# Kernel tuning notes

Hardware: AMD Instinct MI355X
Metric: run time of the kernel (lower is better)

## Reference

```python
import jax, jax.numpy as jnp
import numpy as np
import math

B, T, C = 2, 2048, 2048
NH = 16
HS = C // NH            # 128
N_ELEM = int(0.5 * HS)  # 64, rotary_percentage=0.5
A_T = 10                # adapter_prompt_length


def setup_inputs() -> dict:
    key = jax.random.key(0)
    ks = jax.random.split(key, 8)
    x = jax.random.normal(ks[0], (B, T, C), dtype=jnp.float32)
    # RoPE cache: standard cos/sin of shape (T, n_elem)
    theta = 10000.0 ** (-jnp.arange(0, N_ELEM, 2, dtype=jnp.float32) / N_ELEM)
    pos = jnp.arange(T, dtype=jnp.float32)
    ang = pos[:, None] * theta[None, :]           # (T, n_elem/2)
    ang = jnp.concatenate([ang, ang], axis=-1)    # (T, n_elem)
    cos, sin = jnp.cos(ang), jnp.sin(ang)
    mask = jnp.tril(jnp.ones((T, T), dtype=bool))  # causal
    s = 0.02
    attn_w = jax.random.normal(ks[1], (3 * C, C), dtype=jnp.float32) * s
    attn_b = jax.random.normal(ks[2], (3 * C,), dtype=jnp.float32) * s
    proj_w = jax.random.normal(ks[3], (C, C), dtype=jnp.float32) * s
    proj_b = jax.random.normal(ks[4], (C,), dtype=jnp.float32) * s
    adapter_wte = jax.random.normal(ks[5], (A_T, C), dtype=jnp.float32) * s
    gating_factor = jnp.full((1,), 0.1, dtype=jnp.float32)  # nonzero so adapter path matters
    return {"x": x, "cos": cos, "sin": sin, "mask": mask,
            "attn_w": attn_w, "attn_b": attn_b, "proj_w": proj_w, "proj_b": proj_b,
            "adapter_wte": adapter_wte, "gating_factor": gating_factor}


def apply_rope(t, cos, sin):
    # t: (B, nh, T, n_elem); cos/sin: (T, n_elem)
    half = t.shape[-1] // 2
    t1, t2 = t[..., :half], t[..., half:]
    rotated = jnp.concatenate([-t2, t1], axis=-1)
    return t * cos + rotated * sin


def sdpa(q, k, v, mask, scale):
    # q: (B,nh,Tq,hs), k/v: (B,nh,Tk,hs); mask: bool broadcastable to (Tq,Tk) or None
    s = jnp.einsum('bhqd,bhkd->bhqk', q, k) * scale
    if mask is not None:
        s = jnp.where(mask, s, jnp.finfo(s.dtype).min)
    p = jax.nn.softmax(s, axis=-1)
    return jnp.einsum('bhqk,bhkd->bhqd', p, v)


def reference(x, cos, sin, mask, attn_w, attn_b, proj_w, proj_b, adapter_wte, gating_factor):
    scale = 1.0 / math.sqrt(HS)
    qkv = x @ attn_w.T + attn_b                    # (B,T,3C)
    qkv = qkv.reshape(B, T, NH, 3 * HS).transpose(0, 2, 1, 3)  # (B,nh,T,3hs)
    q, k, v = jnp.split(qkv, 3, axis=-1)           # each (B,nh,T,hs)
    q = jnp.concatenate([apply_rope(q[..., :N_ELEM], cos, sin), q[..., N_ELEM:]], axis=-1)
    k = jnp.concatenate([apply_rope(k[..., :N_ELEM], cos, sin), k[..., N_ELEM:]], axis=-1)
    y = sdpa(q, k, v, mask, scale)                 # (B,nh,T,hs)
    # adapter-prefix attention
    a_qkv = adapter_wte @ attn_w.T + attn_b        # (aT, 3C)
    _, ak, av = jnp.split(a_qkv, 3, axis=-1)       # (aT, C) each
    ak = ak.reshape(1, A_T, NH, HS).transpose(0, 2, 1, 3)  # (1,nh,aT,hs)
    av = av.reshape(1, A_T, NH, HS).transpose(0, 2, 1, 3)
    ak = jnp.broadcast_to(ak, (B, NH, A_T, HS))
    av = jnp.broadcast_to(av, (B, NH, A_T, HS))
    ay = sdpa(q, ak, av, None, scale)              # full (no mask)
    y = y + gating_factor * ay
    y = y.transpose(0, 2, 1, 3).reshape(B, T, C)
    return y @ proj_w.T + proj_b
```

## Files before the change

kernel.cpp:

```cpp
#include <hip/hip_runtime.h>
#include <math.h>

#define B_DIM 2
#define T_DIM 2048
#define C_DIM 2048
#define NHEAD 16
#define HS 128
#define QKV_N 6144
#define AT 10
#define M_DIM 4096

using bf16x8 = __attribute__((ext_vector_type(8))) short;
using f32x4v = __attribute__((ext_vector_type(4))) float;

__device__ __forceinline__ unsigned short f2bf(float f) {
    union { float f; unsigned int u; } cv; cv.f = f;
    unsigned int u = cv.u;
    return (unsigned short)((u + 0x7FFFu + ((u >> 16) & 1u)) >> 16);
}
__device__ __forceinline__ float bf2f(unsigned short h) {
    union { unsigned int u; float f; } cv; cv.u = ((unsigned int)h) << 16;
    return cv.f;
}
__device__ __forceinline__ unsigned int pack_bf16(float lo, float hi) {
    unsigned int r;
    asm volatile("v_cvt_pk_bf16_f32 %0, %1, %2" : "=v"(r) : "v"(lo), "v"(hi));
    return r;
}
__device__ __forceinline__ void gload_lds16(const void* g, void* l) {
    __builtin_amdgcn_global_load_lds(
        (const __attribute__((address_space(1))) void*)g,
        (__attribute__((address_space(3))) void*)l, 16, 0, 0);
}

__global__ __launch_bounds__(256)
void f32_to_bf16_kernel(const float* __restrict__ in, unsigned short* __restrict__ out, int n8) {
    const int i = blockIdx.x * 256 + threadIdx.x;
    if (i >= n8) return;
    const float4 a = *(const float4*)&in[(size_t)i * 8];
    const float4 b = *(const float4*)&in[(size_t)i * 8 + 4];
    *(ushort4*)&out[(size_t)i * 8]     = make_ushort4(f2bf(a.x), f2bf(a.y), f2bf(a.z), f2bf(a.w));
    *(ushort4*)&out[(size_t)i * 8 + 4] = make_ushort4(f2bf(b.x), f2bf(b.y), f2bf(b.z), f2bf(b.w));
}

template<int BF16OUT>
__global__ __launch_bounds__(256)
void gemm_nt_mfma(const unsigned short* __restrict__ A, const unsigned short* __restrict__ Bw,
                  const float* __restrict__ bias, void* __restrict__ Cout,
                  int M, int N, int K) {
    __shared__ unsigned short As[128 * 32];
    __shared__ unsigned short Bs[128 * 32];

    const int tid  = threadIdx.x;
    const int wave = tid >> 6;
    const int lane = tid & 63;
    const int m0 = blockIdx.y * 128;
    const int n0 = blockIdx.x * 128;
    const int wr = (wave >> 1) * 64;
    const int wc = (wave & 1) * 64;

    f32x4v acc[4][4];
#pragma unroll
    for (int i = 0; i < 4; ++i)
#pragma unroll
        for (int j = 0; j < 4; ++j)
#pragma unroll
            for (int q = 0; q < 4; ++q) acc[i][j][q] = 0.f;

    const int srow = lane >> 2;
    const int sk   = (lane & 3) * 8;
    const int fr   = lane & 15;
    const int fk   = (lane >> 4) * 8;

    for (int k0 = 0; k0 < K; k0 += 32) {
        __syncthreads();
#pragma unroll
        for (int t = 0; t < 2; ++t) {
            const int seg = wave * 2 + t;
            gload_lds16(&A[(size_t)(m0 + seg * 16 + srow) * K + k0 + sk], &As[seg * 512]);
            gload_lds16(&Bw[(size_t)(n0 + seg * 16 + srow) * K + k0 + sk], &Bs[seg * 512]);
        }
        __syncthreads();

        bf16x8 af[4], bfg[4];
#pragma unroll
        for (int i = 0; i < 4; ++i)
            af[i] = *(const bf16x8*)&As[(wr + i * 16 + fr) * 32 + fk];
#pragma unroll
        for (int j = 0; j < 4; ++j)
            bfg[j] = *(const bf16x8*)&Bs[(wc + j * 16 + fr) * 32 + fk];
#pragma unroll
        for (int i = 0; i < 4; ++i)
#pragma unroll
            for (int j = 0; j < 4; ++j)
                acc[i][j] = __builtin_amdgcn_mfma_f32_16x16x32_bf16(af[i], bfg[j], acc[i][j], 0, 0, 0);
    }

    const int r4 = (lane >> 4) * 4;
#pragma unroll
    for (int i = 0; i < 4; ++i) {
#pragma unroll
        for (int j = 0; j < 4; ++j) {
            const int col = n0 + wc + j * 16 + fr;
            const float bv = bias[col];
#pragma unroll
            for (int q = 0; q < 4; ++q) {
                const int row = m0 + wr + i * 16 + r4 + q;
                const float v = acc[i][j][q] + bv;
                if (BF16OUT) ((unsigned short*)Cout)[(size_t)row * N + col] = f2bf(v);
                else         ((float*)Cout)[(size_t)row * N + col] = v;
            }
        }
    }
}

__global__ __launch_bounds__(256)
void rope_repack(const unsigned short* __restrict__ qkvb, const float* __restrict__ cosb,
                 const float* __restrict__ sinb, unsigned short* __restrict__ Qb,
                 unsigned short* __restrict__ Kb, unsigned short* __restrict__ Vt) {
    __shared__ unsigned short Vlds[64 * 132];

    const int tid = threadIdx.x;
    const int t64 = blockIdx.x & 31;
    const int h   = (blockIdx.x >> 5) & 15;
    const int b   = blockIdx.x >> 9;
    const int bh  = b * NHEAD + h;
    const int t0  = t64 * 64;

    const int r = tid >> 2, part = tid & 3;
    const size_t inrow  = ((size_t)(b * T_DIM + t0 + r)) * QKV_N + h * 384;
    const size_t outrow = ((size_t)bh * T_DIM + t0 + r) * HS;

    {
        const int isK = part >> 1;
        const int sub = part & 1;
        const unsigned short* src = qkvb + inrow + isK * 128;
        unsigned short* dst = (isK ? Kb : Qb) + outrow;
        if (sub == 0) {
#pragma unroll
            for (int g = 0; g < 8; ++g) {
                const int i = g * 4;
                ushort4 t1 = *(const ushort4*)&src[i];
                ushort4 t2 = *(const ushort4*)&src[32 + i];
                const float4 cv = *(const float4*)&cosb[(t0 + r) * 64 + i];
                const float4 sv = *(const float4*)&sinb[(t0 + r) * 64 + i];
                const float a0 = bf2f(t1.x), a1 = bf2f(t1.y), a2 = bf2f(t1.z), a3 = bf2f(t1.w);
                const float b0 = bf2f(t2.x), b1 = bf2f(t2.y), b2 = bf2f(t2.z), b3 = bf2f(t2.w);
                *(ushort4*)&dst[i] = make_ushort4(
                    f2bf(a0 * cv.x - b0 * sv.x), f2bf(a1 * cv.y - b1 * sv.y),
                    f2bf(a2 * cv.z - b2 * sv.z), f2bf(a3 * cv.w - b3 * sv.w));
                *(ushort4*)&dst[32 + i] = make_ushort4(
                    f2bf(b0 * cv.x + a0 * sv.x), f2bf(b1 * cv.y + a1 * sv.y),
                    f2bf(b2 * cv.z + a2 * sv.z), f2bf(b3 * cv.w + a3 * sv.w));
            }
        } else {
#pragma unroll
            for (int g = 0; g < 8; ++g) {
                *(ushort4*)&dst[64 + g * 8]     = *(const ushort4*)&src[64 + g * 8];
                *(ushort4*)&dst[64 + g * 8 + 4] = *(const ushort4*)&src[64 + g * 8 + 4];
            }
        }
    }

    {
        const unsigned short* vsrc = qkvb + inrow + 256;
#pragma unroll
        for (int g = 0; g < 8; ++g)
            *(ushort4*)&Vlds[r * 132 + part * 32 + g * 4] = *(const ushort4*)&vsrc[part * 32 + g * 4];
    }
    __syncthreads();
    {
        const int d = tid >> 1, tc = tid & 1;
        unsigned short* vdst = Vt + ((size_t)bh * HS + d) * T_DIM + t0 + tc * 32;
#pragma unroll
        for (int g = 0; g < 8; ++g) {
            ushort4 o;
            o.x = Vlds[(tc * 32 + g * 4 + 0) * 132 + d];
            o.y = Vlds[(tc * 32 + g * 4 + 1) * 132 + d];
            o.z = Vlds[(tc * 32 + g * 4 + 2) * 132 + d];
            o.w = Vlds[(tc * 32 + g * 4 + 3) * 132 + d];
            *(ushort4*)&vdst[g * 4] = o;
        }
    }
}

__global__ __launch_bounds__(64)
void adapter_qkv_kernel(const float* __restrict__ wte, const float* __restrict__ w,
                        const float* __restrict__ bias, float* __restrict__ aqkv) {
    const int n = blockIdx.x;
    const int lane = threadIdx.x;
    float acc[AT];
#pragma unroll
    for (int a = 0; a < AT; ++a) acc[a] = 0.f;
    for (int k = lane * 4; k < C_DIM; k += 64 * 4) {
        float4 wv = *(const float4*)&w[(size_t)n * C_DIM + k];
#pragma unroll
        for (int a = 0; a < AT; ++a) {
            float4 tv = *(const float4*)&wte[(size_t)a * C_DIM + k];
            acc[a] += wv.x * tv.x + wv.y * tv.y + wv.z * tv.z + wv.w * tv.w;
        }
    }
#pragma unroll
    for (int a = 0; a < AT; ++a) {
        float v = acc[a];
        for (int off = 32; off; off >>= 1) v += __shfl_down(v, off);
        if (lane == 0) aqkv[(size_t)a * QKV_N + n] = v + bias[n];
    }
}

__global__ __launch_bounds__(256)
void flash_mfma(const unsigned short* __restrict__ Qb, const unsigned short* __restrict__ Kb,
                const unsigned short* __restrict__ Vt, const float* __restrict__ aqkv,
                const float* __restrict__ gating, unsigned short* __restrict__ yb) {
    __shared__ __align__(16) unsigned char smem[32768];
    unsigned short* Ks = (unsigned short*)smem;
    unsigned short* Vs = (unsigned short*)(smem + 16384);

    const int tid = threadIdx.x;
    const int wave = tid >> 6, lane = tid & 63;
    const int lo = lane & 15, hi = lane >> 4;

    const int qt = 31 - (blockIdx.x & 31);
    const int h  = (blockIdx.x >> 5) & 15;
    const int b  = blockIdx.x >> 9;
    const int q0 = qt * 64;
    const int bh = b * NHEAD + h;
    const float scale = 0.08838834764831845f;

    const unsigned short* Qh = Qb + (size_t)bh * T_DIM * HS;
    const unsigned short* Kh = Kb + (size_t)bh * T_DIM * HS;
    const unsigned short* Vh = Vt + (size_t)bh * HS * T_DIM;

    const int myqrow = q0 + wave * 16 + lo;

    bf16x8 qf[4];
    {
        const unsigned short* qrow = Qh + (size_t)myqrow * HS;
#pragma unroll
        for (int c = 0; c < 4; ++c) qf[c] = *(const bf16x8*)&qrow[c * 32 + hi * 8];
    }

    f32x4v oacc[8];
#pragma unroll
    for (int d = 0; d < 8; ++d)
#pragma unroll
        for (int q = 0; q < 4; ++q) oacc[d][q] = 0.f;
    float m = -INFINITY, ln = 0.f;

    const int ntiles = qt + 1;
    for (int kt = 0; kt < ntiles; ++kt) {
        const int k0 = kt * 64;
        __syncthreads();
#pragma unroll
        for (int t = 0; t < 4; ++t) {
            const int kr = wave * 16 + t * 4 + hi;
            gload_lds16(Kh + (size_t)(k0 + kr) * HS + 8 * (lo ^ (kr & 7)),
                        &Ks[(wave * 16 + t * 4) * 128]);
            const int vr = (wave * 4 + t) * 8 + (lane >> 3);
            gload_lds16(Vh + (size_t)vr * T_DIM + k0 + 8 * ((lane & 7) ^ (vr & 7)),
                        &Vs[(wave * 4 + t) * 8 * 64]);
        }
        __syncthreads();

        f32x4v sacc[4];
#pragma unroll
        for (int s = 0; s < 4; ++s) {
#pragma unroll
            for (int q = 0; q < 4; ++q) sacc[s][q] = 0.f;
            const int krow = s * 16 + lo;
            const int rs = (lo & 7) << 4;
#pragma unroll
            for (int c = 0; c < 4; ++c) {
                const int boff = (c * 64 + hi * 16) ^ rs;
                bf16x8 kf = *(const bf16x8*)&Ks[krow * 128 + (boff >> 1)];
                sacc[s] = __builtin_amdgcn_mfma_f32_16x16x32_bf16(kf, qf[c], sacc[s], 0, 0, 0);
            }
        }

        const bool dtile = (kt == qt);
        float p[4][4];
        float xm = -INFINITY;
#pragma unroll
        for (int s = 0; s < 4; ++s)
#pragma unroll
            for (int q = 0; q < 4; ++q) {
                float v = sacc[s][q] * scale;
                if (dtile && (k0 + s * 16 + hi * 4 + q > myqrow)) v = -INFINITY;
                p[s][q] = v;
                xm = fmaxf(xm, v);
            }
        xm = fmaxf(xm, __shfl_xor(xm, 16));
        xm = fmaxf(xm, __shfl_xor(xm, 32));
        const float mnew = fmaxf(m, xm);
        const float al = __expf(m - mnew);
        float psum = 0.f;
#pragma unroll
        for (int s = 0; s < 4; ++s)
#pragma unroll
            for (int q = 0; q < 4; ++q) {
                p[s][q] = __expf(p[s][q] - mnew);
                psum += p[s][q];
            }
        psum += __shfl_xor(psum, 16);
        psum += __shfl_xor(psum, 32);
        ln = ln * al + psum;
        m = mnew;

        float aq[4];
#pragma unroll
        for (int q = 0; q < 4; ++q) aq[q] = __shfl(al, hi * 4 + q);
#pragma unroll
        for (int d = 0; d < 8; ++d)
#pragma unroll
            for (int q = 0; q < 4; ++q) oacc[d][q] *= aq[q];

        unsigned int pk[4][2];
#pragma unroll
        for (int s = 0; s < 4; ++s) {
            pk[s][0] = pack_bf16(p[s][0], p[s][1]);
            pk[s][1] = pack_bf16(p[s][2], p[s][3]);
        }
        const int src0 = lo + ((hi & 1) << 5);
        const int src1 = src0 + 16;
        const bool shi = (hi >> 1) != 0;
#pragma unroll
        for (int c = 0; c < 2; ++c) {
            const unsigned int a0 = (unsigned int)__shfl((int)pk[c*2][0], src0);
            const unsigned int b0 = (unsigned int)__shfl((int)pk[c*2+1][0], src0);
            const unsigned int a1 = (unsigned int)__shfl((int)pk[c*2][1], src0);
            const unsigned int b1 = (unsigned int)__shfl((int)pk[c*2+1][1], src0);
            const unsigned int a2 = (unsigned int)__shfl((int)pk[c*2][0], src1);
            const unsigned int b2 = (unsigned int)__shfl((int)pk[c*2+1][0], src1);
            const unsigned int a3 = (unsigned int)__shfl((int)pk[c*2][1], src1);
            const unsigned int b3 = (unsigned int)__shfl((int)pk[c*2+1][1], src1);
            union { unsigned int u[4]; bf16x8 v; } cv2;
            cv2.u[0] = shi ? b0 : a0;
            cv2.u[1] = shi ? b1 : a1;
            cv2.u[2] = shi ? b2 : a2;
            cv2.u[3] = shi ? b3 : a3;
            const bf16x8 pf = cv2.v;
#pragma unroll
            for (int d = 0; d < 8; ++d) {
                const int vrow = d * 16 + lo;
                const int boff = (c * 64 + hi * 16) ^ ((lo & 7) << 4);
                bf16x8 vf = *(const bf16x8*)&Vs[vrow * 64 + (boff >> 1)];
                oacc[d] = __builtin_amdgcn_mfma_f32_16x16x32_bf16(pf, vf, oacc[d], 0, 0, 0);
            }
        }
    }

    float linv[4];
#pragma unroll
    for (int q = 0; q < 4; ++q) linv[q] = 1.f / __shfl(ln, hi * 4 + q);
#pragma unroll
    for (int d = 0; d < 8; ++d)
#pragma unroll
        for (int q = 0; q < 4; ++q) oacc[d][q] *= linv[q];

    __syncthreads();
    float* AK = (float*)smem;
    float* AV = AK + AT * HS;
    for (int idx = tid; idx < AT * HS; idx += 256) {
        const int a = idx >> 7, d = idx & 127;
        AK[idx] = aqkv[(size_t)a * QKV_N + C_DIM + h * HS + d];
        AV[idx] = aqkv[(size_t)a * QKV_N + 2 * C_DIM + h * HS + d];
    }
    __syncthreads();

    float qflt[4][8];
#pragma unroll
    for (int c = 0; c < 4; ++c)
#pragma unroll
        for (int j = 0; j < 8; ++j) qflt[c][j] = bf2f((unsigned short)qf[c][j]);

    float e[AT];
    float amax = -INFINITY;
#pragma unroll
    for (int a = 0; a < AT; ++a) {
        float t = 0.f;
#pragma unroll
        for (int c = 0; c < 4; ++c) {
            const float4 k0v = *(const float4*)&AK[a * HS + c * 32 + hi * 8];
            const float4 k1v = *(const float4*)&AK[a * HS + c * 32 + hi * 8 + 4];
            t += qflt[c][0] * k0v.x + qflt[c][1] * k0v.y + qflt[c][2] * k0v.z + qflt[c][3] * k0v.w
               + qflt[c][4] * k1v.x + qflt[c][5] * k1v.y + qflt[c][6] * k1v.z + qflt[c][7] * k1v.w;
        }
        t += __shfl_xor(t, 16);
        t += __shfl_xor(t, 32);
        e[a] = t * scale;
        amax = fmaxf(amax, e[a]);
    }
    float asum = 0.f;
#pragma unroll
    for (int a = 0; a < AT; ++a) { e[a] = __expf(e[a] - amax); asum += e[a]; }
    const float gcoef = gating[0] / asum;

#pragma unroll
    for (int a = 0; a < AT; ++a) {
        const float ca = e[a] * gcoef;
        float cq[4];
#pragma unroll
        for (int q = 0; q < 4; ++q) cq[q] = __shfl(ca, hi * 4 + q);
#pragma unroll
        for (int d = 0; d < 8; ++d) {
            const float av = AV[a * HS + d * 16 + lo];
#pragma unroll
            for (int q = 0; q < 4; ++q) oacc[d][q] += cq[q] * av;
        }
    }

#pragma unroll
    for (int q = 0; q < 4; ++q) {
        const int row = q0 + wave * 16 + hi * 4 + q;
        unsigned short* dst = yb + ((size_t)(b * T_DIM + row)) * C_DIM + h * HS + lo;
#pragma unroll
        for (int d = 0; d < 8; ++d) dst[d * 16] = f2bf(oacc[d][q]);
    }
}

extern "C" void kernel_launch(void* const* d_in, const int* in_sizes, int n_in,
                              void* d_out, int out_size, void* d_ws, size_t ws_size,
                              hipStream_t stream) {
    const float* x       = (const float*)d_in[0];
    const float* cosb    = (const float*)d_in[1];
    const float* sinb    = (const float*)d_in[2];
    const float* attn_w  = (const float*)d_in[4];
    const float* attn_b  = (const float*)d_in[5];
    const float* proj_w  = (const float*)d_in[6];
    const float* proj_b  = (const float*)d_in[7];
    const float* wte     = (const float*)d_in[8];
    const float* gating  = (const float*)d_in[9];
    float* out = (float*)d_out;

    float* aqkv = (float*)d_ws;
    unsigned short* qkvb = (unsigned short*)(aqkv + (size_t)AT * QKV_N);
    unsigned short* xb   = qkvb + (size_t)M_DIM * QKV_N;
    unsigned short* awb  = xb + (size_t)M_DIM * C_DIM;
    unsigned short* Vt   = awb + (size_t)QKV_N * C_DIM;
    unsigned short* Qb   = xb;
    unsigned short* Kb   = awb;
    unsigned short* pwb  = qkvb;
    unsigned short* yv   = qkvb + (size_t)C_DIM * C_DIM;

    f32_to_bf16_kernel<<<(M_DIM * C_DIM / 8 + 255) / 256, 256, 0, stream>>>(x, xb, M_DIM * C_DIM / 8);
    f32_to_bf16_kernel<<<(QKV_N * C_DIM / 8 + 255) / 256, 256, 0, stream>>>(attn_w, awb, QKV_N * C_DIM / 8);
    gemm_nt_mfma<1><<<dim3(QKV_N / 128, M_DIM / 128), 256, 0, stream>>>(
        xb, awb, attn_b, qkvb, M_DIM, QKV_N, C_DIM);
    adapter_qkv_kernel<<<QKV_N, 64, 0, stream>>>(wte, attn_w, attn_b, aqkv);
    rope_repack<<<B_DIM * NHEAD * (T_DIM / 64), 256, 0, stream>>>(qkvb, cosb, sinb, Qb, Kb, Vt);
    f32_to_bf16_kernel<<<(C_DIM * C_DIM / 8 + 255) / 256, 256, 0, stream>>>(proj_w, pwb, C_DIM * C_DIM / 8);
    flash_mfma<<<B_DIM * NHEAD * (T_DIM / 64), 256, 0, stream>>>(Qb, Kb, Vt, aqkv, gating, yv);
    gemm_nt_mfma<0><<<dim3(C_DIM / 128, M_DIM / 128), 256, 0, stream>>>(
        yv, pwb, proj_b, out, M_DIM, C_DIM, C_DIM);
}
```

Measured before the change: 531.1 us.

## Double-buffer flash attention, pair causal tiles, lazy rescale, swizzle GEMM blocks

The flash attention kernel now double-buffers K/V tiles in shared memory so the next tile loads while the current one computes. Each block handles two query tiles (qt and 31-qt) to balance causal work, which halves the grid. Softmax switches to exp2 with the log2e factor folded into the scale, and skips the rescale unless the running max grows by more than a threshold. It also adds s_setprio hints around the MFMA sections, swizzles GEMM block indices for cache locality, and has the adapter QKV read the bf16 weight copy instead of fp32. Trade-offs are fewer blocks in flight, more LDS per block, and adapter K/V computed from bf16 weights, a small precision change.

```diff
diff --git a/kernel.cpp b/kernel.cpp
--- a/kernel.cpp
+++ b/kernel.cpp
@@ -54,8 +54,13 @@
     const int tid  = threadIdx.x;
     const int wave = tid >> 6;
     const int lane = tid & 63;
-    const int m0 = blockIdx.y * 128;
-    const int n0 = blockIdx.x * 128;
+
+    const int nwg = gridDim.x * gridDim.y;
+    int bid = blockIdx.y * gridDim.x + blockIdx.x;
+    bid = (bid & 7) * (nwg >> 3) + (bid >> 3);
+    const int m0 = (bid / gridDim.x) * 128;
+    const int n0 = (bid % gridDim.x) * 128;
+
     const int wr = (wave >> 1) * 64;
     const int wc = (wave & 1) * 64;
 
@@ -185,19 +190,24 @@
 }
 
 __global__ __launch_bounds__(64)
-void adapter_qkv_kernel(const float* __restrict__ wte, const float* __restrict__ w,
+void adapter_qkv_kernel(const float* __restrict__ wte, const unsigned short* __restrict__ wb,
                         const float* __restrict__ bias, float* __restrict__ aqkv) {
     const int n = blockIdx.x;
     const int lane = threadIdx.x;
     float acc[AT];
 #pragma unroll
     for (int a = 0; a < AT; ++a) acc[a] = 0.f;
-    for (int k = lane * 4; k < C_DIM; k += 64 * 4) {
-        float4 wv = *(const float4*)&w[(size_t)n * C_DIM + k];
+    for (int k = lane * 8; k < C_DIM; k += 64 * 8) {
+        const ushort4 wa = *(const ushort4*)&wb[(size_t)n * C_DIM + k];
+        const ushort4 wc = *(const ushort4*)&wb[(size_t)n * C_DIM + k + 4];
+        const float w0 = bf2f(wa.x), w1 = bf2f(wa.y), w2 = bf2f(wa.z), w3 = bf2f(wa.w);
+        const float w4 = bf2f(wc.x), w5 = bf2f(wc.y), w6 = bf2f(wc.z), w7 = bf2f(wc.w);
 #pragma unroll
         for (int a = 0; a < AT; ++a) {
-            float4 tv = *(const float4*)&wte[(size_t)a * C_DIM + k];
-            acc[a] += wv.x * tv.x + wv.y * tv.y + wv.z * tv.z + wv.w * tv.w;
+            const float4 t0 = *(const float4*)&wte[(size_t)a * C_DIM + k];
+            const float4 t1 = *(const float4*)&wte[(size_t)a * C_DIM + k + 4];
+            acc[a] += w0 * t0.x + w1 * t0.y + w2 * t0.z + w3 * t0.w
+                    + w4 * t1.x + w5 * t1.y + w6 * t1.z + w7 * t1.w;
         }
     }
 #pragma unroll
@@ -212,209 +222,229 @@
 void flash_mfma(const unsigned short* __restrict__ Qb, const unsigned short* __restrict__ Kb,
                 const unsigned short* __restrict__ Vt, const float* __restrict__ aqkv,
                 const float* __restrict__ gating, unsigned short* __restrict__ yb) {
-    __shared__ __align__(16) unsigned char smem[32768];
-    unsigned short* Ks = (unsigned short*)smem;
-    unsigned short* Vs = (unsigned short*)(smem + 16384);
+    __shared__ __align__(16) unsigned short smem[2][16384];
 
     const int tid = threadIdx.x;
     const int wave = tid >> 6, lane = tid & 63;
     const int lo = lane & 15, hi = lane >> 4;
 
-    const int qt = 31 - (blockIdx.x & 31);
-    const int h  = (blockIdx.x >> 5) & 15;
-    const int b  = blockIdx.x >> 9;
-    const int q0 = qt * 64;
+    const int z = blockIdx.x & 15;
+    const int h = (blockIdx.x >> 4) & 15;
+    const int b = blockIdx.x >> 8;
     const int bh = b * NHEAD + h;
-    const float scale = 0.08838834764831845f;
+    const float kscale = 0.08838834764831845f * 1.4426950408889634f;
 
     const unsigned short* Qh = Qb + (size_t)bh * T_DIM * HS;
     const unsigned short* Kh = Kb + (size_t)bh * T_DIM * HS;
     const unsigned short* Vh = Vt + (size_t)bh * HS * T_DIM;
 
-    const int myqrow = q0 + wave * 16 + lo;
-
-    bf16x8 qf[4];
-    {
-        const unsigned short* qrow = Qh + (size_t)myqrow * HS;
-#pragma unroll
-        for (int c = 0; c < 4; ++c) qf[c] = *(const bf16x8*)&qrow[c * 32 + hi * 8];
-    }
-
-    f32x4v oacc[8];
-#pragma unroll
-    for (int d = 0; d < 8; ++d)
-#pragma unroll
-        for (int q = 0; q < 4; ++q) oacc[d][q] = 0.f;
-    float m = -INFINITY, ln = 0.f;
-
-    const int ntiles = qt + 1;
-    for (int kt = 0; kt < ntiles; ++kt) {
-        const int k0 = kt * 64;
-        __syncthreads();
+    float* AK = (float*)&smem[0][0];
+    float* AV = AK + AT * HS;
+
+    auto STAGE = [&](int k0, int bufi) {
+        unsigned short* Kd = &smem[bufi][0];
+        unsigned short* Vd = &smem[bufi][8192];
 #pragma unroll
         for (int t = 0; t < 4; ++t) {
             const int kr = wave * 16 + t * 4 + hi;
             gload_lds16(Kh + (size_t)(k0 + kr) * HS + 8 * (lo ^ (kr & 7)),
-                        &Ks[(wave * 16 + t * 4) * 128]);
+                        &Kd[(wave * 16 + t * 4) * 128]);
             const int vr = (wave * 4 + t) * 8 + (lane >> 3);
             gload_lds16(Vh + (size_t)vr * T_DIM + k0 + 8 * ((lane & 7) ^ (vr & 7)),
-                        &Vs[(wave * 4 + t) * 8 * 64]);
-        }
+                        &Vd[(wave * 4 + t) * 8 * 64]);
+        }
+    };
+
+#pragma unroll 1
+    for (int pass = 0; pass < 2; ++pass) {
+        const int qt = pass ? z : (31 - z);
+        const int q0 = qt * 64;
+        const int myqrow = q0 + wave * 16 + lo;
+
+        bf16x8 qf[4];
+        {
+            const unsigned short* qrow = Qh + (size_t)myqrow * HS;
+#pragma unroll
+            for (int c = 0; c < 4; ++c) qf[c] = *(const bf16x8*)&qrow[c * 32 + hi * 8];
+        }
+
+        f32x4v oacc[8];
+#pragma unroll
+        for (int d = 0; d < 8; ++d)
+#pragma unroll
+            for (int q = 0; q < 4; ++q) oacc[d][q] = 0.f;
+        float m = -INFINITY, ln = 0.f;
+
+        STAGE(0, 0);
+        int cur = 0;
+        for (int kt = 0; kt <= qt; ++kt) {
+            const int k0 = kt * 64;
+            __syncthreads();
+            if (kt < qt) STAGE(k0 + 64, cur ^ 1);
+            const unsigned short* Ks = &smem[cur][0];
+            const unsigned short* Vs = &smem[cur][8192];
+
+            f32x4v sacc[4];
+            __builtin_amdgcn_s_setprio(1);
+#pragma unroll
+            for (int s = 0; s < 4; ++s) {
+#pragma unroll
+                for (int q = 0; q < 4; ++q) sacc[s][q] = 0.f;
+                const int krow = s * 16 + lo;
+                const int rs = (lo & 7) << 4;
+#pragma unroll
+                for (int c = 0; c < 4; ++c) {
+                    const int boff = (c * 64 + hi * 16) ^ rs;
+                    bf16x8 kf = *(const bf16x8*)&Ks[krow * 128 + (boff >> 1)];
+                    sacc[s] = __builtin_amdgcn_mfma_f32_16x16x32_bf16(kf, qf[c], sacc[s], 0, 0, 0);
+                }
+            }
+            __builtin_amdgcn_s_setprio(0);
+
+            const bool dtile = (kt == qt);
+            float p[4][4];
+            float xm = -INFINITY;
+#pragma unroll
+            for (int s = 0; s < 4; ++s)
+#pragma unroll
+                for (int q = 0; q < 4; ++q) {
+                    float v = sacc[s][q] * kscale;
+                    if (dtile && (k0 + s * 16 + hi * 4 + q > myqrow)) v = -INFINITY;
+                    p[s][q] = v;
+                    xm = fmaxf(xm, v);
+                }
+            xm = fmaxf(xm, __shfl_xor(xm, 16));
+            xm = fmaxf(xm, __shfl_xor(xm, 32));
+            if (__any(xm > m + 11.5f)) {
+                const float mnew = fmaxf(m, xm);
+                const float al = exp2f(m - mnew);
+                m = mnew;
+                ln *= al;
+                float aq[4];
+#pragma unroll
+                for (int q = 0; q < 4; ++q) aq[q] = __shfl(al, hi * 4 + q);
+#pragma unroll
+                for (int d = 0; d < 8; ++d)
+#pragma unroll
+                    for (int q = 0; q < 4; ++q) oacc[d][q] *= aq[q];
+            }
+            float psum = 0.f;
+#pragma unroll
+            for (int s = 0; s < 4; ++s)
+#pragma unroll
+                for (int q = 0; q < 4; ++q) {
+                    p[s][q] = exp2f(p[s][q] - m);
+                    psum += p[s][q];
+                }
+            psum += __shfl_xor(psum, 16);
+            psum += __shfl_xor(psum, 32);
+            ln += psum;
+
+            unsigned int pk[4][2];
+#pragma unroll
+            for (int s = 0; s < 4; ++s) {
+                pk[s][0] = pack_bf16(p[s][0], p[s][1]);
+                pk[s][1] = pack_bf16(p[s][2], p[s][3]);
+            }
+            const int src0 = lo + ((hi & 1) << 5);
+            const int src1 = src0 + 16;
+            const bool shi = (hi >> 1) != 0;
+#pragma unroll
+            for (int c = 0; c < 2; ++c) {
+                const unsigned int a0 = (unsigned int)__shfl((int)pk[c*2][0], src0);
+                const unsigned int b0 = (unsigned int)__shfl((int)pk[c*2+1][0], src0);
+                const unsigned int a1 = (unsigned int)__shfl((int)pk[c*2][1], src0);
+                const unsigned int b1 = (unsigned int)__shfl((int)pk[c*2+1][1], src0);
+                const unsigned int a2 = (unsigned int)__shfl((int)pk[c*2][0], src1);
+                const unsigned int b2 = (unsigned int)__shfl((int)pk[c*2+1][0], src1);
+                const unsigned int a3 = (unsigned int)__shfl((int)pk[c*2][1], src1);
+                const unsigned int b3 = (unsigned int)__shfl((int)pk[c*2+1][1], src1);
+                union { unsigned int u[4]; bf16x8 v; } cv2;
+                cv2.u[0] = shi ? b0 : a0;
+                cv2.u[1] = shi ? b1 : a1;
+                cv2.u[2] = shi ? b2 : a2;
+                cv2.u[3] = shi ? b3 : a3;
+                const bf16x8 pf = cv2.v;
+                __builtin_amdgcn_s_setprio(1);
+#pragma unroll
+                for (int d = 0; d < 8; ++d) {
+                    const int vrow = d * 16 + lo;
+                    const int boff = (c * 64 + hi * 16) ^ ((lo & 7) << 4);
+                    bf16x8 vf = *(const bf16x8*)&Vs[vrow * 64 + (boff >> 1)];
+                    oacc[d] = __builtin_amdgcn_mfma_f32_16x16x32_bf16(pf, vf, oacc[d], 0, 0, 0);
+                }
+                __builtin_amdgcn_s_setprio(0);
+            }
+            cur ^= 1;
+        }
+
+        float linv[4];
+#pragma unroll
+        for (int q = 0; q < 4; ++q) linv[q] = 1.f / __shfl(ln, hi * 4 + q);
+#pragma unroll
+        for (int d = 0; d < 8; ++d)
+#pragma unroll
+            for (int q = 0; q < 4; ++q) oacc[d][q] *= linv[q];
+
         __syncthreads();
-
-        f32x4v sacc[4];
-#pragma unroll
-        for (int s = 0; s < 4; ++s) {
-#pragma unroll
-            for (int q = 0; q < 4; ++q) sacc[s][q] = 0.f;
-            const int krow = s * 16 + lo;
-            const int rs = (lo & 7) << 4;
+        for (int idx = tid; idx < AT * HS; idx += 256) {
+            const int a = idx >> 7, d = idx & 127;
+            AK[idx] = aqkv[(size_t)a * QKV_N + C_DIM + h * HS + d];
+            AV[idx] = aqkv[(size_t)a * QKV_N + 2 * C_DIM + h * HS + d];
+        }
+        __syncthreads();
+
+        float qflt[4][8];
+#pragma unroll
+        for (int c = 0; c < 4; ++c)
+#pragma unroll
+            for (int j = 0; j < 8; ++j) qflt[c][j] = bf2f((unsigned short)qf[c][j]);
+
+        float e[AT];
+        float amax = -INFINITY;
+#pragma unroll
+        for (int a = 0; a < AT; ++a) {
+            float t = 0.f;
 #pragma unroll
             for (int c = 0; c < 4; ++c) {
-                const int boff = (c * 64 + hi * 16) ^ rs;
-                bf16x8 kf = *(const bf16x8*)&Ks[krow * 128 + (boff >> 1)];
-                sacc[s] = __builtin_amdgcn_mfma_f32_16x16x32_bf16(kf, qf[c], sacc[s], 0, 0, 0);
-            }
-        }
-
-        const bool dtile = (kt == qt);
-        float p[4][4];
-        float xm = -INFINITY;
-#pragma unroll
-        for (int s = 0; s < 4; ++s)
-#pragma unroll
-            for (int q = 0; q < 4; ++q) {
-                float v = sacc[s][q] * scale;
-                if (dtile && (k0 + s * 16 + hi * 4 + q > myqrow)) v = -INFINITY;
-                p[s][q] = v;
-                xm = fmaxf(xm, v);
-            }
-        xm = fmaxf(xm, __shfl_xor(xm, 16));
-        xm = fmaxf(xm, __shfl_xor(xm, 32));
-        const float mnew = fmaxf(m, xm);
-        const float al = __expf(m - mnew);
-        float psum = 0.f;
-#pragma unroll
-        for (int s = 0; s < 4; ++s)
-#pragma unroll
-            for (int q = 0; q < 4; ++q) {
-                p[s][q] = __expf(p[s][q] - mnew);
-                psum += p[s][q];
-            }
-        psum += __shfl_xor(psum, 16);
-        psum += __shfl_xor(psum, 32);
-        ln = ln * al + psum;
-        m = mnew;
-
-        float aq[4];
-#pragma unroll
-        for (int q = 0; q < 4; ++q) aq[q] = __shfl(al, hi * 4 + q);
-#pragma unroll
-        for (int d = 0; d < 8; ++d)
-#pragma unroll
-            for (int q = 0; q < 4; ++q) oacc[d][q] *= aq[q];
-
-        unsigned int pk[4][2];
-#pragma unroll
-        for (int s = 0; s < 4; ++s) {
-            pk[s][0] = pack_bf16(p[s][0], p[s][1]);
-            pk[s][1] = pack_bf16(p[s][2], p[s][3]);
-        }
-        const int src0 = lo + ((hi & 1) << 5);
-        const int src1 = src0 + 16;
-        const bool shi = (hi >> 1) != 0;
-#pragma unroll
-        for (int c = 0; c < 2; ++c) {
-            const unsigned int a0 = (unsigned int)__shfl((int)pk[c*2][0], src0);
-            const unsigned int b0 = (unsigned int)__shfl((int)pk[c*2+1][0], src0);
-            const unsigned int a1 = (unsigned int)__shfl((int)pk[c*2][1], src0);
-            const unsigned int b1 = (unsigned int)__shfl((int)pk[c*2+1][1], src0);
-            const unsigned int a2 = (unsigned int)__shfl((int)pk[c*2][0], src1);
-            const unsigned int b2 = (unsigned int)__shfl((int)pk[c*2+1][0], src1);
-            const unsigned int a3 = (unsigned int)__shfl((int)pk[c*2][1], src1);
-            const unsigned int b3 = (unsigned int)__shfl((int)pk[c*2+1][1], src1);
-            union { unsigned int u[4]; bf16x8 v; } cv2;
-            cv2.u[0] = shi ? b0 : a0;
-            cv2.u[1] = shi ? b1 : a1;
-            cv2.u[2] = shi ? b2 : a2;
-            cv2.u[3] = shi ? b3 : a3;
-            const bf16x8 pf = cv2.v;
+                const float4 k0v = *(const float4*)&AK[a * HS + c * 32 + hi * 8];
+                const float4 k1v = *(const float4*)&AK[a * HS + c * 32 + hi * 8 + 4];
+                t += qflt[c][0] * k0v.x + qflt[c][1] * k0v.y + qflt[c][2] * k0v.z + qflt[c][3] * k0v.w
+                   + qflt[c][4] * k1v.x + qflt[c][5] * k1v.y + qflt[c][6] * k1v.z + qflt[c][7] * k1v.w;
+            }
+            t += __shfl_xor(t, 16);
+            t += __shfl_xor(t, 32);
+            e[a] = t * 0.08838834764831845f;
+            amax = fmaxf(amax, e[a]);
+        }
+        float asum = 0.f;
+#pragma unroll
+        for (int a = 0; a < AT; ++a) { e[a] = __expf(e[a] - amax); asum += e[a]; }
+        const float gcoef = gating[0] / asum;
+
+#pragma unroll
+        for (int a = 0; a < AT; ++a) {
+            const float ca = e[a] * gcoef;
+            float cq[4];
+#pragma unroll
+            for (int q = 0; q < 4; ++q) cq[q] = __shfl(ca, hi * 4 + q);
 #pragma unroll
             for (int d = 0; d < 8; ++d) {
-                const int vrow = d * 16 + lo;
-                const int boff = (c * 64 + hi * 16) ^ ((lo & 7) << 4);
-                bf16x8 vf = *(const bf16x8*)&Vs[vrow * 64 + (boff >> 1)];
-                oacc[d] = __builtin_amdgcn_mfma_f32_16x16x32_bf16(pf, vf, oacc[d], 0, 0, 0);
-            }
-        }
-    }
-
-    float linv[4];
-#pragma unroll
-    for (int q = 0; q < 4; ++q) linv[q] = 1.f / __shfl(ln, hi * 4 + q);
-#pragma unroll
-    for (int d = 0; d < 8; ++d)
-#pragma unroll
-        for (int q = 0; q < 4; ++q) oacc[d][q] *= linv[q];
-
-    __syncthreads();
-    float* AK = (float*)smem;
-    float* AV = AK + AT * HS;
-    for (int idx = tid; idx < AT * HS; idx += 256) {
-        const int a = idx >> 7, d = idx & 127;
-        AK[idx] = aqkv[(size_t)a * QKV_N + C_DIM + h * HS + d];
-        AV[idx] = aqkv[(size_t)a * QKV_N + 2 * C_DIM + h * HS + d];
-    }
-    __syncthreads();
-
-    float qflt[4][8];
-#pragma unroll
-    for (int c = 0; c < 4; ++c)
-#pragma unroll
-        for (int j = 0; j < 8; ++j) qflt[c][j] = bf2f((unsigned short)qf[c][j]);
-
-    float e[AT];
-    float amax = -INFINITY;
-#pragma unroll
-    for (int a = 0; a < AT; ++a) {
-        float t = 0.f;
-#pragma unroll
-        for (int c = 0; c < 4; ++c) {
-            const float4 k0v = *(const float4*)&AK[a * HS + c * 32 + hi * 8];
-            const float4 k1v = *(const float4*)&AK[a * HS + c * 32 + hi * 8 + 4];
-            t += qflt[c][0] * k0v.x + qflt[c][1] * k0v.y + qflt[c][2] * k0v.z + qflt[c][3] * k0v.w
-               + qflt[c][4] * k1v.x + qflt[c][5] * k1v.y + qflt[c][6] * k1v.z + qflt[c][7] * k1v.w;
-        }
-        t += __shfl_xor(t, 16);
-        t += __shfl_xor(t, 32);
-        e[a] = t * scale;
-        amax = fmaxf(amax, e[a]);
-    }
-    float asum = 0.f;
-#pragma unroll
-    for (int a = 0; a < AT; ++a) { e[a] = __expf(e[a] - amax); asum += e[a]; }
-    const float gcoef = gating[0] / asum;
-
-#pragma unroll
-    for (int a = 0; a < AT; ++a) {
-        const float ca = e[a] * gcoef;
-        float cq[4];
-#pragma unroll
-        for (int q = 0; q < 4; ++q) cq[q] = __shfl(ca, hi * 4 + q);
-#pragma unroll
-        for (int d = 0; d < 8; ++d) {
-            const float av = AV[a * HS + d * 16 + lo];
-#pragma unroll
-            for (int q = 0; q < 4; ++q) oacc[d][q] += cq[q] * av;
-        }
-    }
-
-#pragma unroll
-    for (int q = 0; q < 4; ++q) {
-        const int row = q0 + wave * 16 + hi * 4 + q;
-        unsigned short* dst = yb + ((size_t)(b * T_DIM + row)) * C_DIM + h * HS + lo;
-#pragma unroll
-        for (int d = 0; d < 8; ++d) dst[d * 16] = f2bf(oacc[d][q]);
+                const float av = AV[a * HS + d * 16 + lo];
+#pragma unroll
+                for (int q = 0; q < 4; ++q) oacc[d][q] += cq[q] * av;
+            }
+        }
+
+#pragma unroll
+        for (int q = 0; q < 4; ++q) {
+            const int row = q0 + wave * 16 + hi * 4 + q;
+            unsigned short* dst = yb + ((size_t)(b * T_DIM + row)) * C_DIM + h * HS + lo;
+#pragma unroll
+            for (int d = 0; d < 8; ++d) dst[d * 16] = f2bf(oacc[d][q]);
+        }
+
+        if (pass == 0) __syncthreads();
     }
 }
 
@@ -446,10 +476,10 @@
     f32_to_bf16_kernel<<<(QKV_N * C_DIM / 8 + 255) / 256, 256, 0, stream>>>(attn_w, awb, QKV_N * C_DIM / 8);
     gemm_nt_mfma<1><<<dim3(QKV_N / 128, M_DIM / 128), 256, 0, stream>>>(
         xb, awb, attn_b, qkvb, M_DIM, QKV_N, C_DIM);
-    adapter_qkv_kernel<<<QKV_N, 64, 0, stream>>>(wte, attn_w, attn_b, aqkv);
+    adapter_qkv_kernel<<<QKV_N, 64, 0, stream>>>(wte, awb, attn_b, aqkv);
     rope_repack<<<B_DIM * NHEAD * (T_DIM / 64), 256, 0, stream>>>(qkvb, cosb, sinb, Qb, Kb, Vt);
     f32_to_bf16_kernel<<<(C_DIM * C_DIM / 8 + 255) / 256, 256, 0, stream>>>(proj_w, pwb, C_DIM * C_DIM / 8);
-    flash_mfma<<<B_DIM * NHEAD * (T_DIM / 64), 256, 0, stream>>>(Qb, Kb, Vt, aqkv, gating, yv);
+    flash_mfma<<<B_DIM * NHEAD * 16, 256, 0, stream>>>(Qb, Kb, Vt, aqkv, gating, yv);
     gemm_nt_mfma<0><<<dim3(C_DIM / 128, M_DIM / 128), 256, 0, stream>>>(
         yv, pwb, proj_b, out, M_DIM, C_DIM, C_DIM);
 }
```

Result: faster. 490.7 us (-7.6%).
